# Optimization experiments

Hardware: AMD Instinct MI355X
Metric: run time of the kernel (lower is better)

The kernel has to match this reference:

```python
import jax, jax.numpy as jnp
import numpy as np

B, D, V = 128, 4096, 32000


def setup_inputs() -> dict:
    key = jax.random.key(0)
    k1, k2, k3, k4 = jax.random.split(key, 4)
    hidden_states = jax.random.normal(k1, (B, D), dtype=jnp.float32)
    embd_weight = jax.random.normal(k2, (V, D), dtype=jnp.float32) * 0.02
    # per-row temperature in [0.5, 1.5), top_p in [0.7, 1.0)
    temperature = jax.random.uniform(k3, (B,), jnp.float32, 0.5, 1.5)
    top_p = jax.random.uniform(k4, (B,), jnp.float32, 0.7, 1.0)
    return {"hidden_states": hidden_states, "embd_weight": embd_weight,
            "temperature": temperature, "top_p": top_p}


def _topp_logits(hidden_states, embd_weight, temperature, top_p):
    # [B, V] logits via tied LM head
    logits = jnp.einsum('bd,vd->bv', hidden_states, embd_weight)
    logits = logits / temperature[:, None]
    # descending sort (matches torch sort(descending=True))
    order = jnp.argsort(-logits, axis=-1)                    # [B, V]
    sorted_logits = jnp.take_along_axis(logits, order, axis=-1)
    sorted_probs = jax.nn.softmax(sorted_logits, axis=-1)
    cum = jnp.cumsum(sorted_probs, axis=-1)
    # mask tokens whose preceding cumulative prob already exceeds top_p
    mask = (cum - sorted_probs) > top_p[:, None]
    sorted_logits = jnp.where(mask, -jnp.inf, sorted_logits)
    inv = jnp.argsort(order, axis=-1)                        # undo the sort
    return jnp.take_along_axis(sorted_logits, inv, axis=-1)


def reference(hidden_states, embd_weight, temperature, top_p):
    logits = _topp_logits(hidden_states, embd_weight, temperature, top_p)
    probs = jax.nn.softmax(logits.astype(jnp.float32), axis=-1)
    # multinomial(num_samples=1) == categorical sample per row (fixed key for determinism)
    ids = jax.random.categorical(jax.random.key(42), jnp.log(probs), axis=-1)
    return ids
```

## Files before the change

### kernel.cpp

```cpp
#include <hip/hip_runtime.h>
#include <math.h>

#define B_ 128
#define D_ 4096
#define V_ 32000

#define BN 64
#define BK 32
#define KSTEPS (D_ / BK)
#define ASTEP_BYTES (128 * BK * 2 * 2)
#define ASTEP_SHORTS (ASTEP_BYTES / 2)
#define WS_LDS_BYTES (2 * 4 * 4 * 16 * 16)
#define WS_LDS_OFF ASTEP_BYTES

#define SCALE_A 256.0f
#define SCALE_W 4096.0f
#define DESCALE 9.5367431640625e-7f

typedef __attribute__((ext_vector_type(8))) short short8;
typedef __attribute__((ext_vector_type(8))) _Float16 half8;
typedef __attribute__((ext_vector_type(4))) float floatx4;

__device__ __forceinline__ void threefry2x32_0_42(unsigned& x0, unsigned& x1) {
  const unsigned k0 = 0u;
  const unsigned k1 = 42u;
  const unsigned k2 = 0u ^ 42u ^ 0x1BD11BDAu;
  x0 += k0; x1 += k1;
#define TF_R(r) { x0 += x1; x1 = (x1 << (r)) | (x1 >> (32 - (r))); x1 ^= x0; }
#define TF_G0 TF_R(13) TF_R(15) TF_R(26) TF_R(6)
#define TF_G1 TF_R(17) TF_R(29) TF_R(16) TF_R(24)
  TF_G0; x0 += k1; x1 += k2 + 1u;
  TF_G1; x0 += k2; x1 += k0 + 2u;
  TF_G0; x0 += k0; x1 += k1 + 3u;
  TF_G1; x0 += k1; x1 += k2 + 4u;
  TF_G0; x0 += k2; x1 += k0 + 5u;
#undef TF_G1
#undef TF_G0
#undef TF_R
}

__device__ __forceinline__ float gumbel_from_bits(unsigned bits) {
  float f = __uint_as_float((bits >> 9) | 0x3F800000u) - 1.0f;
  float u = fmaxf(f, 1.17549435e-38f);
  return -logf(-logf(u));
}

__global__ __launch_bounds__(256) void asplit_kernel(const float* __restrict__ A,
                                                     unsigned short* __restrict__ Asp) {
  const int t = blockIdx.x * 256 + threadIdx.x;
  const int m_glob = t >> 9;
  const int koct = t & 511;
  const int sk = koct >> 2, quad = koct & 3;
  const int mt = m_glob >> 4, ml = m_glob & 15;
  const float* src = A + (size_t)m_glob * D_ + koct * 8;
  half8 h0, h1;
#pragma unroll
  for (int kk = 0; kk < 8; kk++) {
    const float x = src[kk] * SCALE_A;
    const _Float16 a0 = (_Float16)x;
    const float r1 = x - (float)a0;
    const _Float16 a1 = (_Float16)r1;
    h0[kk] = a0; h1[kk] = a1;
  }
  unsigned short* dst = Asp + (size_t)sk * ASTEP_SHORTS;
  const int base = ((mt * 4 + quad) * 16 + ml) * 8;
  const int sstride = 8 * 4 * 16 * 8;
  *(half8*)(dst + base) = h0;
  *(half8*)(dst + base + sstride) = h1;
}

__global__ __launch_bounds__(256) void gemm_mfma(const unsigned short* __restrict__ Asp,
                                                 const float* __restrict__ W,
                                                 const float* __restrict__ temp,
                                                 float* __restrict__ L) {
  __shared__ unsigned char lds[ASTEP_BYTES + WS_LDS_BYTES];
  const int tid = threadIdx.x;
  const int vblock = blockIdx.x * BN;
  const int wave = tid >> 6, lane = tid & 63;
  const int quad = lane >> 4, ml = lane & 15;
  const int wm = wave >> 1, wn = wave & 1;

  const int wv = tid >> 2;
  const int wko = tid & 3;
  const float* wsrc = W + (size_t)(vblock + wv) * D_ + wko * 8;
  const int wnt = wv >> 4, wvl = wv & 15;
  const int wbase0 = WS_LDS_OFF + (((0 * 4 + wnt) * 4 + wko) * 16 + wvl) * 16;
  const int wsstride = 4 * 4 * 16 * 16;

  floatx4 acc[4][2];
#pragma unroll
  for (int i = 0; i < 4; i++)
#pragma unroll
    for (int j = 0; j < 2; j++) acc[i][j] = (floatx4){0.f, 0.f, 0.f, 0.f};

  float4 wa = *(const float4*)(wsrc);
  float4 wb = *(const float4*)(wsrc + 4);

  for (int st = 0; st < KSTEPS; st++) {
    __syncthreads();
    const unsigned char* abase = (const unsigned char*)(Asp + (size_t)st * ASTEP_SHORTS);
#pragma unroll
    for (int i = 0; i < 4; i++) {
      const int off = (i * 256 + tid) * 16;
      __builtin_amdgcn_global_load_lds(
          (const __attribute__((address_space(1))) unsigned int*)(abase + off),
          (__attribute__((address_space(3))) unsigned int*)(&lds[off]), 16, 0, 0);
    }
    {
      const float x[8] = {wa.x, wa.y, wa.z, wa.w, wb.x, wb.y, wb.z, wb.w};
      half8 w0, w1;
#pragma unroll
      for (int kk = 0; kk < 8; kk++) {
        const float xs = x[kk] * SCALE_W;
        const _Float16 b0 = (_Float16)xs;
        const float r1 = xs - (float)b0;
        const _Float16 b1 = (_Float16)r1;
        w0[kk] = b0; w1[kk] = b1;
      }
      *(half8*)(&lds[wbase0]) = w0;
      *(half8*)(&lds[wbase0 + wsstride]) = w1;
    }
    {
      const int stn = (st + 1 < KSTEPS) ? st + 1 : st;
      const float* wp = wsrc + (size_t)stn * BK;
      wa = *(const float4*)(wp);
      wb = *(const float4*)(wp + 4);
    }
    __syncthreads();

    half8 af[2][4];
#pragma unroll
    for (int s = 0; s < 2; s++)
#pragma unroll
      for (int i = 0; i < 4; i++) {
        const int mt = wm * 4 + i;
        af[s][i] = *(const half8*)(&lds[(((s * 8 + mt) * 4 + quad) * 16 + ml) * 16]);
      }
    half8 wf[2][2];
#pragma unroll
    for (int s = 0; s < 2; s++)
#pragma unroll
      for (int j = 0; j < 2; j++) {
        const int nt = wn * 2 + j;
        wf[s][j] = *(const half8*)(&lds[WS_LDS_OFF + (((s * 4 + nt) * 4 + quad) * 16 + ml) * 16]);
      }

#pragma unroll
    for (int i = 0; i < 4; i++)
#pragma unroll
      for (int j = 0; j < 2; j++) {
        acc[i][j] = __builtin_amdgcn_mfma_f32_16x16x32_f16(af[0][i], wf[0][j], acc[i][j], 0, 0, 0);
        acc[i][j] = __builtin_amdgcn_mfma_f32_16x16x32_f16(af[0][i], wf[1][j], acc[i][j], 0, 0, 0);
        acc[i][j] = __builtin_amdgcn_mfma_f32_16x16x32_f16(af[1][i], wf[0][j], acc[i][j], 0, 0, 0);
        acc[i][j] = __builtin_amdgcn_mfma_f32_16x16x32_f16(af[1][i], wf[1][j], acc[i][j], 0, 0, 0);
      }
  }

#pragma unroll
  for (int i = 0; i < 4; i++)
#pragma unroll
    for (int j = 0; j < 2; j++) {
      const int col = vblock + (wn * 2 + j) * 16 + ml;
#pragma unroll
      for (int r = 0; r < 4; r++) {
        const int row = wm * 64 + i * 16 + quad * 4 + r;
        L[(size_t)row * V_ + col] = acc[i][j][r] * (DESCALE / temp[row]);
      }
    }
}

#define NBINS 8192
#define SHIFT 17
#define CAP 2048

__device__ __forceinline__ float blockSum1024(float x, float* redf) {
#pragma unroll
  for (int o = 32; o > 0; o >>= 1) x += __shfl_down(x, o);
  const int w = threadIdx.x >> 6;
  __syncthreads();
  if ((threadIdx.x & 63) == 0) redf[w] = x;
  __syncthreads();
  if (threadIdx.x == 0) {
    float t = redf[0];
    for (int k = 1; k < 16; k++) t += redf[k];
    redf[16] = t;
  }
  __syncthreads();
  return redf[16];
}

__device__ __forceinline__ float blockMax1024(float x, float* redf) {
#pragma unroll
  for (int o = 32; o > 0; o >>= 1) x = fmaxf(x, __shfl_down(x, o));
  const int w = threadIdx.x >> 6;
  __syncthreads();
  if ((threadIdx.x & 63) == 0) redf[w] = x;
  __syncthreads();
  if (threadIdx.x == 0) {
    float t = redf[0];
    for (int k = 1; k < 16; k++) t = fmaxf(t, redf[k]);
    redf[16] = t;
  }
  __syncthreads();
  return redf[16];
}

__global__ __launch_bounds__(1024) void sampler_kernel(const float* __restrict__ L,
                                                       const float* __restrict__ top_p,
                                                       int* __restrict__ out) {
  __shared__ float hist[NBINS];
  __shared__ float listE[CAP];
  __shared__ int cnt;
  __shared__ float redf[20];
  __shared__ int redi[16];
  const int b = blockIdx.x, tid = threadIdx.x;
  const float* l = L + (size_t)b * V_;

  for (int i = tid; i < NBINS; i += 1024) hist[i] = 0.f;
  if (tid == 0) cnt = 0;
  __syncthreads();

  float mx = -INFINITY;
  for (int v = tid; v < V_; v += 1024) mx = fmaxf(mx, l[v]);
  mx = blockMax1024(mx, redf);

  float s = 0.f;
  for (int v = tid; v < V_; v += 1024) {
    const float e = expf(l[v] - mx);
    s += e;
    unsigned bin = __float_as_uint(e) >> SHIFT;
    if (bin >= NBINS) bin = NBINS - 1;
    atomicAdd(&hist[bin], e);
  }
  const float S = blockSum1024(s, redf);
  const float ps = top_p[b] * S;

  int lo = -1, hi = NBINS - 1;
  while (hi - lo > 1) {
    const int mid = (lo + hi) >> 1;
    float a = 0.f;
    for (int i = tid; i < NBINS; i += 1024)
      if (i > mid) a += hist[i];
    a = blockSum1024(a, redf);
    if (a <= ps) hi = mid; else lo = mid;
  }
  const int beta = hi;
  float cumAbove;
  {
    float a = 0.f;
    for (int i = tid; i < NBINS; i += 1024)
      if (i > beta) a += hist[i];
    cumAbove = blockSum1024(a, redf);
  }

  for (int v = tid; v < V_; v += 1024) {
    const float e = expf(l[v] - mx);
    unsigned bin = __float_as_uint(e) >> SHIFT;
    if (bin >= NBINS) bin = NBINS - 1;
    if ((int)bin == beta) {
      const int p = atomicAdd(&cnt, 1);
      if (p < CAP) listE[p] = e;
    }
  }
  __syncthreads();
  const int n = cnt;

  long long blo = ((long long)beta << SHIFT) - 1;
  long long bhi = ((long long)(beta + 1)) << SHIFT;
  if (n <= CAP) {
    while (bhi - blo > 1) {
      const long long mid = (blo + bhi) >> 1;
      const float t = __uint_as_float((unsigned)mid);
      float a = 0.f;
      for (int i = tid; i < n; i += 1024) {
        const float e = listE[i];
        if (e > t) a += e;
      }
      a = cumAbove + blockSum1024(a, redf);
      if (a <= ps) bhi = mid; else blo = mid;
    }
  } else {
    while (bhi - blo > 1) {
      const long long mid = (blo + bhi) >> 1;
      const float t = __uint_as_float((unsigned)mid);
      float a = 0.f;
      for (int v = tid; v < V_; v += 1024) {
        const float e = expf(l[v] - mx);
        unsigned bin = __float_as_uint(e) >> SHIFT;
        if (bin >= NBINS) bin = NBINS - 1;
        if ((int)bin == beta && e > t) a += e;
      }
      a = cumAbove + blockSum1024(a, redf);
      if (a <= ps) bhi = mid; else blo = mid;
    }
  }
  const unsigned c = (unsigned)bhi;

  float best = -INFINITY;
  int bi = 0x7FFFFFFF;
  for (int v = tid; v < V_; v += 1024) {
    const float lv = l[v];
    const float e = expf(lv - mx);
    if (__float_as_uint(e) >= c) {
      unsigned x0 = 0u, x1 = (unsigned)(b * V_ + v);
      threefry2x32_0_42(x0, x1);
      const float sc = lv + gumbel_from_bits(x0 ^ x1);
      if (sc > best) { best = sc; bi = v; }
    }
  }
#pragma unroll
  for (int o = 32; o > 0; o >>= 1) {
    const float t = __shfl_down(best, o);
    const int j = __shfl_down(bi, o);
    if (t > best || (t == best && j < bi)) { best = t; bi = j; }
  }
  const int w = tid >> 6;
  __syncthreads();
  if ((tid & 63) == 0) { redf[w] = best; redi[w] = bi; }
  __syncthreads();
  if (tid == 0) {
    float bs = redf[0];
    int bidx = redi[0];
    for (int k = 1; k < 16; k++)
      if (redf[k] > bs || (redf[k] == bs && redi[k] < bidx)) { bs = redf[k]; bidx = redi[k]; }
    out[b] = bidx;
  }
}

extern "C" void kernel_launch(void* const* d_in, const int* in_sizes, int n_in,
                              void* d_out, int out_size, void* d_ws, size_t ws_size,
                              hipStream_t stream) {
  (void)in_sizes; (void)n_in; (void)out_size; (void)ws_size;
  const float* A = (const float*)d_in[0];
  const float* W = (const float*)d_in[1];
  const float* temp = (const float*)d_in[2];
  const float* topp = (const float*)d_in[3];
  int* out = (int*)d_out;

  char* base = (char*)d_ws;
  float* L = (float*)base;
  unsigned short* Asp = (unsigned short*)(base + (size_t)B_ * V_ * 4);

  asplit_kernel<<<dim3(256), dim3(256), 0, stream>>>(A, Asp);
  gemm_mfma<<<dim3(V_ / BN), dim3(256), 0, stream>>>(Asp, W, temp, L);
  sampler_kernel<<<dim3(B_), dim3(1024), 0, stream>>>(L, topp, out);
}
```

Measured before the change: 871.9 us.

## Double-buffer LDS in the split-fp16 GEMM to overlap loads with MFMA

Turns the single-buffered LDS staging of the logits GEMM into a two-buffer ping-pong pipeline. While one buffer is consumed by MFMA, the next K-step's A tile is loaded asynchronously and the split W tile is written into the other buffer. This drops one of the two barriers per K-step and overlaps global and LDS traffic with compute. In exchange it doubles LDS use per block, which may lower occupancy, and the loop is unrolled manually with an explicit prologue and epilogue.

```diff
diff --git a/kernel.cpp b/kernel.cpp
--- a/kernel.cpp
+++ b/kernel.cpp
@@ -12,14 +12,16 @@
 #define ASTEP_SHORTS (ASTEP_BYTES / 2)
 #define WS_LDS_BYTES (2 * 4 * 4 * 16 * 16)
 #define WS_LDS_OFF ASTEP_BYTES
+#define BUF_STRIDE (ASTEP_BYTES + WS_LDS_BYTES)
 
 #define SCALE_A 256.0f
 #define SCALE_W 4096.0f
 #define DESCALE 9.5367431640625e-7f
 
-typedef __attribute__((ext_vector_type(8))) short short8;
 typedef __attribute__((ext_vector_type(8))) _Float16 half8;
 typedef __attribute__((ext_vector_type(4))) float floatx4;
+
+#define MFMA16(a, b, c) __builtin_amdgcn_mfma_f32_16x16x32_f16((a), (b), (c), 0, 0, 0)
 
 __device__ __forceinline__ void threefry2x32_0_42(unsigned& x0, unsigned& x1) {
   const unsigned k0 = 0u;
@@ -73,7 +75,7 @@
                                                  const float* __restrict__ W,
                                                  const float* __restrict__ temp,
                                                  float* __restrict__ L) {
-  __shared__ unsigned char lds[ASTEP_BYTES + WS_LDS_BYTES];
+  __shared__ unsigned char lds[2 * BUF_STRIDE];
   const int tid = threadIdx.x;
   const int vblock = blockIdx.x * BN;
   const int wave = tid >> 6, lane = tid & 63;
@@ -84,7 +86,7 @@
   const int wko = tid & 3;
   const float* wsrc = W + (size_t)(vblock + wv) * D_ + wko * 8;
   const int wnt = wv >> 4, wvl = wv & 15;
-  const int wbase0 = WS_LDS_OFF + (((0 * 4 + wnt) * 4 + wko) * 16 + wvl) * 16;
+  const int wbase0 = WS_LDS_OFF + ((wnt * 4 + wko) * 16 + wvl) * 16;
   const int wsstride = 4 * 4 * 16 * 16;
 
   floatx4 acc[4][2];
@@ -93,12 +95,71 @@
 #pragma unroll
     for (int j = 0; j < 2; j++) acc[i][j] = (floatx4){0.f, 0.f, 0.f, 0.f};
 
-  float4 wa = *(const float4*)(wsrc);
-  float4 wb = *(const float4*)(wsrc + 4);
-
-  for (int st = 0; st < KSTEPS; st++) {
-    __syncthreads();
-    const unsigned char* abase = (const unsigned char*)(Asp + (size_t)st * ASTEP_SHORTS);
+#define WSPLIT_STORE(WA, WB, BUFN_)                                            \
+  {                                                                            \
+    const float x[8] = {WA.x, WA.y, WA.z, WA.w, WB.x, WB.y, WB.z, WB.w};       \
+    half8 w0, w1;                                                              \
+    _Pragma("unroll") for (int kk = 0; kk < 8; kk++) {                         \
+      const float xs = x[kk] * SCALE_W;                                        \
+      const _Float16 b0 = (_Float16)xs;                                        \
+      const float r1 = xs - (float)b0;                                         \
+      w0[kk] = b0; w1[kk] = (_Float16)r1;                                      \
+    }                                                                          \
+    *(half8*)(&lds[(BUFN_)*BUF_STRIDE + wbase0]) = w0;                         \
+    *(half8*)(&lds[(BUFN_)*BUF_STRIDE + wbase0 + wsstride]) = w1;              \
+  }
+
+#define COMPUTE(BUFC_)                                                         \
+  {                                                                            \
+    half8 af[2][4];                                                            \
+    _Pragma("unroll") for (int s = 0; s < 2; s++)                              \
+    _Pragma("unroll") for (int i = 0; i < 4; i++) {                            \
+      const int mt = wm * 4 + i;                                               \
+      af[s][i] = *(const half8*)(&lds[(BUFC_)*BUF_STRIDE +                     \
+                    (((s * 8 + mt) * 4 + quad) * 16 + ml) * 16]);              \
+    }                                                                          \
+    half8 wf[2][2];                                                            \
+    _Pragma("unroll") for (int s = 0; s < 2; s++)                              \
+    _Pragma("unroll") for (int j = 0; j < 2; j++) {                            \
+      const int nt = wn * 2 + j;                                               \
+      wf[s][j] = *(const half8*)(&lds[(BUFC_)*BUF_STRIDE + WS_LDS_OFF +        \
+                    (((s * 4 + nt) * 4 + quad) * 16 + ml) * 16]);              \
+    }                                                                          \
+    _Pragma("unroll") for (int i = 0; i < 4; i++)                              \
+    _Pragma("unroll") for (int j = 0; j < 2; j++) {                            \
+      acc[i][j] = MFMA16(af[0][i], wf[0][j], acc[i][j]);                       \
+      acc[i][j] = MFMA16(af[0][i], wf[1][j], acc[i][j]);                       \
+      acc[i][j] = MFMA16(af[1][i], wf[0][j], acc[i][j]);                       \
+      acc[i][j] = MFMA16(af[1][i], wf[1][j], acc[i][j]);                       \
+    }                                                                          \
+  }
+
+#define GSTEP(BUFC_, BUFN_, WCA, WCB, WNA, WNB, TSTAGE, TPREF, DO_PREF)        \
+  {                                                                            \
+    const unsigned char* abase =                                               \
+        (const unsigned char*)(Asp + (size_t)(TSTAGE) * ASTEP_SHORTS);         \
+    _Pragma("unroll") for (int i = 0; i < 4; i++) {                            \
+      const int off = (i * 256 + tid) * 16;                                    \
+      __builtin_amdgcn_global_load_lds(                                        \
+          (const __attribute__((address_space(1))) unsigned int*)(abase + off),\
+          (__attribute__((address_space(3))) unsigned int*)(                   \
+              &lds[(BUFN_)*BUF_STRIDE + off]), 16, 0, 0);                      \
+    }                                                                          \
+    if (DO_PREF) {                                                             \
+      const float* wp = wsrc + (size_t)(TPREF) * BK;                           \
+      WNA = *(const float4*)(wp);                                              \
+      WNB = *(const float4*)(wp + 4);                                          \
+    }                                                                          \
+    WSPLIT_STORE(WCA, WCB, BUFN_);                                             \
+    COMPUTE(BUFC_);                                                            \
+    __syncthreads();                                                           \
+  }
+
+  float4 wa0 = *(const float4*)(wsrc);
+  float4 wb0 = *(const float4*)(wsrc + 4);
+  float4 wa1, wb1;
+  {
+    const unsigned char* abase = (const unsigned char*)Asp;
 #pragma unroll
     for (int i = 0; i < 4; i++) {
       const int off = (i * 256 + tid) * 16;
@@ -106,55 +167,22 @@
           (const __attribute__((address_space(1))) unsigned int*)(abase + off),
           (__attribute__((address_space(3))) unsigned int*)(&lds[off]), 16, 0, 0);
     }
-    {
-      const float x[8] = {wa.x, wa.y, wa.z, wa.w, wb.x, wb.y, wb.z, wb.w};
-      half8 w0, w1;
-#pragma unroll
-      for (int kk = 0; kk < 8; kk++) {
-        const float xs = x[kk] * SCALE_W;
-        const _Float16 b0 = (_Float16)xs;
-        const float r1 = xs - (float)b0;
-        const _Float16 b1 = (_Float16)r1;
-        w0[kk] = b0; w1[kk] = b1;
-      }
-      *(half8*)(&lds[wbase0]) = w0;
-      *(half8*)(&lds[wbase0 + wsstride]) = w1;
-    }
-    {
-      const int stn = (st + 1 < KSTEPS) ? st + 1 : st;
-      const float* wp = wsrc + (size_t)stn * BK;
-      wa = *(const float4*)(wp);
-      wb = *(const float4*)(wp + 4);
-    }
-    __syncthreads();
-
-    half8 af[2][4];
-#pragma unroll
-    for (int s = 0; s < 2; s++)
-#pragma unroll
-      for (int i = 0; i < 4; i++) {
-        const int mt = wm * 4 + i;
-        af[s][i] = *(const half8*)(&lds[(((s * 8 + mt) * 4 + quad) * 16 + ml) * 16]);
-      }
-    half8 wf[2][2];
-#pragma unroll
-    for (int s = 0; s < 2; s++)
-#pragma unroll
-      for (int j = 0; j < 2; j++) {
-        const int nt = wn * 2 + j;
-        wf[s][j] = *(const half8*)(&lds[WS_LDS_OFF + (((s * 4 + nt) * 4 + quad) * 16 + ml) * 16]);
-      }
-
-#pragma unroll
-    for (int i = 0; i < 4; i++)
-#pragma unroll
-      for (int j = 0; j < 2; j++) {
-        acc[i][j] = __builtin_amdgcn_mfma_f32_16x16x32_f16(af[0][i], wf[0][j], acc[i][j], 0, 0, 0);
-        acc[i][j] = __builtin_amdgcn_mfma_f32_16x16x32_f16(af[0][i], wf[1][j], acc[i][j], 0, 0, 0);
-        acc[i][j] = __builtin_amdgcn_mfma_f32_16x16x32_f16(af[1][i], wf[0][j], acc[i][j], 0, 0, 0);
-        acc[i][j] = __builtin_amdgcn_mfma_f32_16x16x32_f16(af[1][i], wf[1][j], acc[i][j], 0, 0, 0);
-      }
-  }
+    WSPLIT_STORE(wa0, wb0, 0);
+    wa0 = *(const float4*)(wsrc + BK);
+    wb0 = *(const float4*)(wsrc + BK + 4);
+  }
+  __syncthreads();
+
+  for (int t2 = 0; t2 < 63; t2++) {
+    const int t = 2 * t2;
+    GSTEP(0, 1, wa0, wb0, wa1, wb1, t + 1, t + 2, 1);
+    GSTEP(1, 0, wa1, wb1, wa0, wb0, t + 2, t + 3, 1);
+  }
+  GSTEP(0, 1, wa0, wb0, wa1, wb1, 127, 127, 0);
+  COMPUTE(1);
+#undef GSTEP
+#undef COMPUTE
+#undef WSPLIT_STORE
 
 #pragma unroll
   for (int i = 0; i < 4; i++)
```

Result: faster. 815.3 us (-6.5%).
